# Performance work log

Hardware: AMD Instinct MI355X
Metric: run time of the kernel (lower is better)

The kernel has to match this reference:

```python
import jax, jax.numpy as jnp
import numpy as np

EMBED_DIM = 512

def setup_inputs() -> dict:
    key = jax.random.key(0)
    ks = jax.random.split(key, 8)
    B, N, M, C = 4, 4096, 4096, EMBED_DIM
    s = 1.0 / np.sqrt(C)
    return {
        "rgb_features": jax.random.normal(ks[0], (B, N, C), jnp.float32),
        "depth_features": jax.random.normal(ks[1], (B, M, C), jnp.float32),
        "Wq": jax.random.normal(ks[2], (C, C), jnp.float32) * s,
        "bq": jnp.zeros((C,), jnp.float32),
        "Wk": jax.random.normal(ks[3], (C, C), jnp.float32) * s,
        "bk": jnp.zeros((C,), jnp.float32),
        "Wv": jax.random.normal(ks[4], (C, C), jnp.float32) * s,
        "bv": jnp.zeros((C,), jnp.float32),
    }

def reference(rgb_features, depth_features, Wq, bq, Wk, bk, Wv, bv):
    C = rgb_features.shape[-1]
    scale = C ** (-0.5)
    Q = rgb_features @ Wq + bq          # [B, N, C]
    K = depth_features @ Wk + bk        # [B, M, C]
    V = depth_features @ Wv + bv        # [B, M, C]
    scores = jnp.einsum('bnc,bmc->bnm', Q, K) * scale
    attn = jax.nn.softmax(scores, axis=-1)
    return jnp.einsum('bnm,bmc->bnc', attn, V)
```

## Files before the change

kernel.cpp:

```cpp
#include <hip/hip_runtime.h>
#include <hip/hip_bf16.h>
#include <stdint.h>


typedef unsigned short u16;
typedef __attribute__((ext_vector_type(8))) short bf16x8;
typedef __attribute__((ext_vector_type(4))) float f32x4;
typedef __attribute__((ext_vector_type(4))) unsigned short u16x4;

#define GLD_LDS16(g, l)                                                        \
  __builtin_amdgcn_global_load_lds(                                            \
      (const __attribute__((address_space(1))) unsigned int*)(g),              \
      (__attribute__((address_space(3))) unsigned int*)(l), 16, 0, 0)

__device__ __forceinline__ u16 f2bf(float f) {
  unsigned x = __float_as_uint(f);
  return (u16)((x + 0x7fffu + ((x >> 16) & 1u)) >> 16);
}

template <int BIAS_MODE, bool OUT_F32, bool SCALE_EN>
__global__ __launch_bounds__(256) void gemm_bt(
    const u16* __restrict__ A, const u16* __restrict__ Bm,
    const float* __restrict__ bias, void* __restrict__ Cv, int M, int N, int K,
    long long sAb, long long sBb, long long sCb, float scale) {
  const int bz = blockIdx.z;
  A += (size_t)bz * sAb;
  Bm += (size_t)bz * sBb;

  const int bm = blockIdx.y * 128;
  const int bn = blockIdx.x * 128;

  __shared__ u16 As[128 * 32];
  __shared__ u16 Bs[128 * 32];

  const int tid = threadIdx.x;
  const int wave = tid >> 6;
  const int lane = tid & 63;
  const int ln = lane & 15;
  const int q = lane >> 4;
  const int wr = wave >> 1;
  const int wc = wave & 1;

  const int rowA = lane >> 2;
  const int ce = (lane & 3) * 8;

  f32x4 acc[4][4] = {};

  for (int k0 = 0; k0 < K; k0 += 32) {
    __syncthreads();
#pragma unroll
    for (int r = 0; r < 2; ++r) {
      const int rb = (r * 4 + wave) * 16;
      GLD_LDS16(A + (size_t)(bm + rb + rowA) * K + k0 + ce, As + rb * 32);
      GLD_LDS16(Bm + (size_t)(bn + rb + rowA) * K + k0 + ce, Bs + rb * 32);
    }
    __syncthreads();

    bf16x8 af[4], bfv[4];
#pragma unroll
    for (int t = 0; t < 4; ++t)
      af[t] = *(const bf16x8*)&As[(wr * 64 + t * 16 + ln) * 32 + q * 8];
#pragma unroll
    for (int u = 0; u < 4; ++u)
      bfv[u] = *(const bf16x8*)&Bs[(wc * 64 + u * 16 + ln) * 32 + q * 8];

#pragma unroll
    for (int t = 0; t < 4; ++t)
#pragma unroll
      for (int u = 0; u < 4; ++u)
        acc[t][u] = __builtin_amdgcn_mfma_f32_16x16x32_bf16(af[t], bfv[u],
                                                            acc[t][u], 0, 0, 0);
  }

  const int crow0 = bm + wr * 64 + q * 4;
  const int ccol0 = bn + wc * 64 + ln;
#pragma unroll
  for (int t = 0; t < 4; ++t) {
#pragma unroll
    for (int u = 0; u < 4; ++u) {
#pragma unroll
      for (int r = 0; r < 4; ++r) {
        const int row = crow0 + t * 16 + r;
        const int col = ccol0 + u * 16;
        float v = acc[t][u][r];
        if constexpr (SCALE_EN) v *= scale;
        if constexpr (BIAS_MODE == 1) v += bias[col];
        if constexpr (BIAS_MODE == 2) v += bias[row];
        const size_t idx = (size_t)bz * (size_t)sCb + (size_t)row * N + col;
        if constexpr (OUT_F32)
          ((float*)Cv)[idx] = v;
        else
          ((u16*)Cv)[idx] = f2bf(v);
      }
    }
  }
}

__global__ __launch_bounds__(256) void cvt_pair(const float* __restrict__ x,
                                                const float* __restrict__ y,
                                                u16* __restrict__ ox,
                                                u16* __restrict__ oy, int n4) {
  const int i = blockIdx.x * 256 + threadIdx.x;
  if (i >= n4) return;
  const float4 a = ((const float4*)x)[i];
  const float4 b = ((const float4*)y)[i];
  u16x4 oa, ob;
  oa[0] = f2bf(a.x); oa[1] = f2bf(a.y); oa[2] = f2bf(a.z); oa[3] = f2bf(a.w);
  ob[0] = f2bf(b.x); ob[1] = f2bf(b.y); ob[2] = f2bf(b.z); ob[3] = f2bf(b.w);
  ((u16x4*)ox)[i] = oa;
  ((u16x4*)oy)[i] = ob;
}

__global__ __launch_bounds__(256) void wtrans_k(const float* __restrict__ W,
                                                u16* __restrict__ WT) {
  const int tr = blockIdx.y * 64;
  const int tc = blockIdx.x * 64;
  __shared__ float T[64][65];
  const int t = threadIdx.x;
  const int r0 = t >> 4;
  const int c0 = (t & 15) * 4;
#pragma unroll
  for (int rr = 0; rr < 4; ++rr) {
    const int row = rr * 16 + r0;
    const float4 w = *(const float4*)&W[(size_t)(tr + row) * 512 + tc + c0];
    T[row][c0 + 0] = w.x; T[row][c0 + 1] = w.y;
    T[row][c0 + 2] = w.z; T[row][c0 + 3] = w.w;
  }
  __syncthreads();
#pragma unroll
  for (int rr = 0; rr < 4; ++rr) {
    const int orow = rr * 16 + r0;
    u16x4 o;
#pragma unroll
    for (int j = 0; j < 4; ++j) o[j] = f2bf(T[c0 + j][orow]);
    *(u16x4*)&WT[(size_t)(tc + orow) * 512 + tr + c0] = o;
  }
}

__global__ __launch_bounds__(256) void softmax_rows(u16* __restrict__ S,
                                                    int cols) {
  u16* p = S + (size_t)blockIdx.x * (size_t)cols;
  const int tid = threadIdx.x;
  const int lane = tid & 63;
  const int wave = tid >> 6;

  uint4 d[2];
  d[0] = ((const uint4*)p)[tid];
  d[1] = ((const uint4*)p)[tid + 256];

  float v[16];
#pragma unroll
  for (int i = 0; i < 2; ++i) {
    const unsigned* w = (const unsigned*)&d[i];
#pragma unroll
    for (int j = 0; j < 4; ++j) {
      v[i * 8 + j * 2 + 0] = __uint_as_float(w[j] << 16);
      v[i * 8 + j * 2 + 1] = __uint_as_float(w[j] & 0xffff0000u);
    }
  }

  float mx = -3.4e38f;
#pragma unroll
  for (int i = 0; i < 16; ++i) mx = fmaxf(mx, v[i]);
#pragma unroll
  for (int o = 32; o > 0; o >>= 1) mx = fmaxf(mx, __shfl_xor(mx, o, 64));

  __shared__ float red[4];
  if (lane == 0) red[wave] = mx;
  __syncthreads();
  mx = fmaxf(fmaxf(red[0], red[1]), fmaxf(red[2], red[3]));

  float s = 0.f;
#pragma unroll
  for (int i = 0; i < 16; ++i) {
    v[i] = __expf(v[i] - mx);
    s += v[i];
  }
#pragma unroll
  for (int o = 32; o > 0; o >>= 1) s += __shfl_xor(s, o, 64);
  __syncthreads();
  if (lane == 0) red[wave] = s;
  __syncthreads();
  s = (red[0] + red[1]) + (red[2] + red[3]);
  const float inv = 1.0f / s;

  uint4 o4[2];
#pragma unroll
  for (int i = 0; i < 2; ++i) {
    unsigned* w = (unsigned*)&o4[i];
#pragma unroll
    for (int j = 0; j < 4; ++j) {
      const unsigned lo = f2bf(v[i * 8 + j * 2 + 0] * inv);
      const unsigned hi = f2bf(v[i * 8 + j * 2 + 1] * inv);
      w[j] = lo | (hi << 16);
    }
  }
  ((uint4*)p)[tid] = o4[0];
  ((uint4*)p)[tid + 256] = o4[1];
}

extern "C" void kernel_launch(void* const* d_in, const int* in_sizes, int n_in,
                              void* d_out, int out_size, void* d_ws,
                              size_t ws_size, hipStream_t stream) {
  const float* rgb = (const float*)d_in[0];
  const float* dep = (const float*)d_in[1];
  const float* Wq = (const float*)d_in[2];
  const float* bq = (const float*)d_in[3];
  const float* Wk = (const float*)d_in[4];
  const float* bk = (const float*)d_in[5];
  const float* Wv = (const float*)d_in[6];
  const float* bv = (const float*)d_in[7];
  float* out = (float*)d_out;

  const int B = 4, N = 4096, M = 4096, C = 512;
  const size_t nBNC = (size_t)B * N * C;
  const float scale = 0.044194173824159216f;

  char* ws = (char*)d_ws;
  size_t off = 0;
  auto carve = [&](size_t bytes) -> void* {
    void* p = ws + off;
    off += (bytes + 255) & ~(size_t)255;
    return p;
  };
  u16* rgb_bf = (u16*)carve(nBNC * 2);
  u16* dep_bf = (u16*)carve(nBNC * 2);
  u16* WqT = (u16*)carve((size_t)C * C * 2);
  u16* WkT = (u16*)carve((size_t)C * C * 2);
  u16* WvT = (u16*)carve((size_t)C * C * 2);
  u16* Qb = (u16*)carve(nBNC * 2);
  u16* Kb = (u16*)carve(nBNC * 2);
  u16* Vt = (u16*)carve(nBNC * 2);
  const size_t base = off;
  const size_t sFull = (size_t)B * N * M * 2;
  const size_t sOne = (size_t)N * M * 2;
  const bool full = ws_size >= base + sFull;
  u16* Sb = (u16*)carve(full ? sFull : sOne);

  cvt_pair<<<8192, 256, 0, stream>>>(rgb, dep, rgb_bf, dep_bf, (int)(nBNC / 4));
  wtrans_k<<<dim3(8, 8), 256, 0, stream>>>(Wq, WqT);
  wtrans_k<<<dim3(8, 8), 256, 0, stream>>>(Wk, WkT);
  wtrans_k<<<dim3(8, 8), 256, 0, stream>>>(Wv, WvT);

  gemm_bt<1, false, false><<<dim3(4, 128, 1), 256, 0, stream>>>(
      rgb_bf, WqT, bq, Qb, 16384, 512, 512, 0, 0, 0, 1.f);
  gemm_bt<1, false, false><<<dim3(4, 128, 1), 256, 0, stream>>>(
      dep_bf, WkT, bk, Kb, 16384, 512, 512, 0, 0, 0, 1.f);
  gemm_bt<2, false, false><<<dim3(32, 4, 4), 256, 0, stream>>>(
      WvT, dep_bf, bv, Vt, 512, 4096, 512, 0, (long long)N * C,
      (long long)C * M, 1.f);

  const long long strQ = (long long)N * C;
  const long long strS = (long long)N * M;
  const long long strV = (long long)C * M;

  if (full) {
    gemm_bt<0, false, true><<<dim3(32, 32, 4), 256, 0, stream>>>(
        Qb, Kb, nullptr, Sb, 4096, 4096, 512, strQ, strQ, strS, scale);
    softmax_rows<<<16384, 256, 0, stream>>>(Sb, 4096);
    gemm_bt<0, true, false><<<dim3(4, 32, 4), 256, 0, stream>>>(
        Sb, Vt, nullptr, out, 4096, 512, 4096, strS, strV, strQ, 1.f);
  } else {
    for (int b = 0; b < 4; ++b) {
      gemm_bt<0, false, true><<<dim3(32, 32, 1), 256, 0, stream>>>(
          Qb + (size_t)b * strQ, Kb + (size_t)b * strQ, nullptr, Sb, 4096, 4096,
          512, 0, 0, 0, scale);
      softmax_rows<<<4096, 256, 0, stream>>>(Sb, 4096);
      gemm_bt<0, true, false><<<dim3(4, 32, 1), 256, 0, stream>>>(
          Sb, Vt + (size_t)b * strV, nullptr, out + (size_t)b * strQ, 4096, 512,
          4096, 0, 0, 0, 1.f);
    }
  }
}
```

Before: 445.8 us.

## Switch GEMMs to 32x32x16 MFMA with swizzled LDS and 256-row QK tiles

Rewrites the shared GEMM kernel to use 32x32x16 bf16 MFMA instructions instead of 16x16x32, which halves the fragment loads per MFMA. An XOR swizzle on the LDS column chunks is added to avoid bank conflicts on the fragment reads. The QK^T score GEMM gets a 256-row tile template, and launch bounds request 2 blocks per CU. The larger tile and accumulator footprint raise register pressure and may limit occupancy.

```diff
diff --git a/kernel.cpp b/kernel.cpp
--- a/kernel.cpp
+++ b/kernel.cpp
@@ -5,7 +5,7 @@
 
 typedef unsigned short u16;
 typedef __attribute__((ext_vector_type(8))) short bf16x8;
-typedef __attribute__((ext_vector_type(4))) float f32x4;
+typedef __attribute__((ext_vector_type(16))) float f32x16;
 typedef __attribute__((ext_vector_type(4))) unsigned short u16x4;
 
 #define GLD_LDS16(g, l)                                                        \
@@ -18,71 +18,86 @@
   return (u16)((x + 0x7fffu + ((x >> 16) & 1u)) >> 16);
 }
 
-template <int BIAS_MODE, bool OUT_F32, bool SCALE_EN>
-__global__ __launch_bounds__(256) void gemm_bt(
+template <int TM, int BIAS_MODE, bool OUT_F32, bool SCALE_EN>
+__global__ __launch_bounds__(256, 2) void gemm32(
     const u16* __restrict__ A, const u16* __restrict__ Bm,
     const float* __restrict__ bias, void* __restrict__ Cv, int M, int N, int K,
     long long sAb, long long sBb, long long sCb, float scale) {
+  constexpr int MSUB = TM / 64;
   const int bz = blockIdx.z;
   A += (size_t)bz * sAb;
   Bm += (size_t)bz * sBb;
 
-  const int bm = blockIdx.y * 128;
+  const int bm = blockIdx.y * TM;
   const int bn = blockIdx.x * 128;
 
-  __shared__ u16 As[128 * 32];
+  __shared__ u16 As[TM * 32];
   __shared__ u16 Bs[128 * 32];
 
   const int tid = threadIdx.x;
   const int wave = tid >> 6;
   const int lane = tid & 63;
-  const int ln = lane & 15;
-  const int q = lane >> 4;
+  const int ln31 = lane & 31;
+  const int half = lane >> 5;
   const int wr = wave >> 1;
   const int wc = wave & 1;
 
   const int rowA = lane >> 2;
-  const int ce = (lane & 3) * 8;
-
-  f32x4 acc[4][4] = {};
+  const int swz = ((lane & 3) ^ (rowA & 3)) * 8;
+
+  f32x16 acc[MSUB][2] = {};
 
   for (int k0 = 0; k0 < K; k0 += 32) {
     __syncthreads();
 #pragma unroll
+    for (int r = 0; r < MSUB; ++r) {
+      const int ch = wave * MSUB + r;
+      GLD_LDS16(A + (size_t)(bm + ch * 16 + rowA) * K + k0 + swz,
+                As + ch * 16 * 32);
+    }
+#pragma unroll
     for (int r = 0; r < 2; ++r) {
-      const int rb = (r * 4 + wave) * 16;
-      GLD_LDS16(A + (size_t)(bm + rb + rowA) * K + k0 + ce, As + rb * 32);
-      GLD_LDS16(Bm + (size_t)(bn + rb + rowA) * K + k0 + ce, Bs + rb * 32);
+      const int ch = wave * 2 + r;
+      GLD_LDS16(Bm + (size_t)(bn + ch * 16 + rowA) * K + k0 + swz,
+                Bs + ch * 16 * 32);
     }
     __syncthreads();
 
-    bf16x8 af[4], bfv[4];
-#pragma unroll
-    for (int t = 0; t < 4; ++t)
-      af[t] = *(const bf16x8*)&As[(wr * 64 + t * 16 + ln) * 32 + q * 8];
-#pragma unroll
-    for (int u = 0; u < 4; ++u)
-      bfv[u] = *(const bf16x8*)&Bs[(wc * 64 + u * 16 + ln) * 32 + q * 8];
-
-#pragma unroll
-    for (int t = 0; t < 4; ++t)
-#pragma unroll
-      for (int u = 0; u < 4; ++u)
-        acc[t][u] = __builtin_amdgcn_mfma_f32_16x16x32_bf16(af[t], bfv[u],
-                                                            acc[t][u], 0, 0, 0);
-  }
-
-  const int crow0 = bm + wr * 64 + q * 4;
-  const int ccol0 = bn + wc * 64 + ln;
-#pragma unroll
-  for (int t = 0; t < 4; ++t) {
-#pragma unroll
-    for (int u = 0; u < 4; ++u) {
-#pragma unroll
-      for (int r = 0; r < 4; ++r) {
-        const int row = crow0 + t * 16 + r;
-        const int col = ccol0 + u * 16;
-        float v = acc[t][u][r];
+#pragma unroll
+    for (int kc = 0; kc < 2; ++kc) {
+      bf16x8 af[MSUB], bfv[2];
+#pragma unroll
+      for (int mt = 0; mt < MSUB; ++mt) {
+        const int row = wr * (MSUB * 32) + mt * 32 + ln31;
+        const int p = (kc * 2 + half) ^ (row & 3);
+        af[mt] = *(const bf16x8*)&As[row * 32 + p * 8];
+      }
+#pragma unroll
+      for (int nt = 0; nt < 2; ++nt) {
+        const int row = wc * 64 + nt * 32 + ln31;
+        const int p = (kc * 2 + half) ^ (row & 3);
+        bfv[nt] = *(const bf16x8*)&Bs[row * 32 + p * 8];
+      }
+#pragma unroll
+      for (int mt = 0; mt < MSUB; ++mt)
+#pragma unroll
+        for (int nt = 0; nt < 2; ++nt)
+          acc[mt][nt] = __builtin_amdgcn_mfma_f32_32x32x16_bf16(
+              af[mt], bfv[nt], acc[mt][nt], 0, 0, 0);
+    }
+  }
+
+  const int crow0 = bm + wr * (MSUB * 32) + 4 * half;
+  const int ccol0 = bn + wc * 64 + ln31;
+#pragma unroll
+  for (int mt = 0; mt < MSUB; ++mt) {
+#pragma unroll
+    for (int nt = 0; nt < 2; ++nt) {
+      const int col = ccol0 + nt * 32;
+#pragma unroll
+      for (int r = 0; r < 16; ++r) {
+        const int row = crow0 + mt * 32 + (r & 3) + 8 * (r >> 2);
+        float v = acc[mt][nt][r];
         if constexpr (SCALE_EN) v *= scale;
         if constexpr (BIAS_MODE == 1) v += bias[col];
         if constexpr (BIAS_MODE == 2) v += bias[row];
@@ -242,31 +257,30 @@
   wtrans_k<<<dim3(8, 8), 256, 0, stream>>>(Wk, WkT);
   wtrans_k<<<dim3(8, 8), 256, 0, stream>>>(Wv, WvT);
 
-  gemm_bt<1, false, false><<<dim3(4, 128, 1), 256, 0, stream>>>(
-      rgb_bf, WqT, bq, Qb, 16384, 512, 512, 0, 0, 0, 1.f);
-  gemm_bt<1, false, false><<<dim3(4, 128, 1), 256, 0, stream>>>(
-      dep_bf, WkT, bk, Kb, 16384, 512, 512, 0, 0, 0, 1.f);
-  gemm_bt<2, false, false><<<dim3(32, 4, 4), 256, 0, stream>>>(
-      WvT, dep_bf, bv, Vt, 512, 4096, 512, 0, (long long)N * C,
-      (long long)C * M, 1.f);
-
   const long long strQ = (long long)N * C;
   const long long strS = (long long)N * M;
   const long long strV = (long long)C * M;
 
+  gemm32<128, 1, false, false><<<dim3(4, 128, 1), 256, 0, stream>>>(
+      rgb_bf, WqT, bq, Qb, 16384, 512, 512, 0, 0, 0, 1.f);
+  gemm32<128, 1, false, false><<<dim3(4, 128, 1), 256, 0, stream>>>(
+      dep_bf, WkT, bk, Kb, 16384, 512, 512, 0, 0, 0, 1.f);
+  gemm32<128, 2, false, false><<<dim3(32, 4, 4), 256, 0, stream>>>(
+      WvT, dep_bf, bv, Vt, 512, 4096, 512, 0, strQ, strV, 1.f);
+
   if (full) {
-    gemm_bt<0, false, true><<<dim3(32, 32, 4), 256, 0, stream>>>(
+    gemm32<256, 0, false, true><<<dim3(32, 16, 4), 256, 0, stream>>>(
         Qb, Kb, nullptr, Sb, 4096, 4096, 512, strQ, strQ, strS, scale);
     softmax_rows<<<16384, 256, 0, stream>>>(Sb, 4096);
-    gemm_bt<0, true, false><<<dim3(4, 32, 4), 256, 0, stream>>>(
+    gemm32<128, 0, true, false><<<dim3(4, 32, 4), 256, 0, stream>>>(
         Sb, Vt, nullptr, out, 4096, 512, 4096, strS, strV, strQ, 1.f);
   } else {
     for (int b = 0; b < 4; ++b) {
-      gemm_bt<0, false, true><<<dim3(32, 32, 1), 256, 0, stream>>>(
+      gemm32<256, 0, false, true><<<dim3(32, 16, 1), 256, 0, stream>>>(
           Qb + (size_t)b * strQ, Kb + (size_t)b * strQ, nullptr, Sb, 4096, 4096,
           512, 0, 0, 0, scale);
       softmax_rows<<<4096, 256, 0, stream>>>(Sb, 4096);
-      gemm_bt<0, true, false><<<dim3(4, 32, 1), 256, 0, stream>>>(
+      gemm32<128, 0, true, false><<<dim3(4, 32, 1), 256, 0, stream>>>(
           Sb, Vt + (size_t)b * strV, nullptr, out + (size_t)b * strQ, 4096, 512,
           4096, 0, 0, 0, 1.f);
     }
```

Measured after the change: 456.0 us. 2.3% more time.
